# Kernel tuning notes

Measured on AMD Instinct MI355X. Metric: run time of the kernel, lower is better.

## Reference

```python
import jax, jax.numpy as jnp
import numpy as np

N_NODES = 100000
N_EDGES = 1600000
D_IN = 128
D_HID = 128
D_OUT = 128


def setup_inputs() -> dict:
    key = jax.random.key(0)
    ks = jax.random.split(key, 6)
    node_features = jax.random.normal(ks[0], (N_NODES, D_IN), dtype=jnp.float32)
    edge_index = jax.random.randint(ks[1], (2, N_EDGES), 0, N_NODES, dtype=jnp.int32)
    s1 = 1.0 / np.sqrt(D_IN)
    s2 = 1.0 / np.sqrt(D_HID)
    W1 = jax.random.normal(ks[2], (D_IN, D_HID), dtype=jnp.float32) * s1
    W2 = jax.random.normal(ks[3], (D_HID, D_HID), dtype=jnp.float32) * s2
    W3 = jax.random.normal(ks[4], (D_HID, D_OUT), dtype=jnp.float32) * s2
    b1 = jnp.zeros((D_HID,), dtype=jnp.float32)
    b2 = jnp.zeros((D_HID,), dtype=jnp.float32)
    b3 = jnp.zeros((D_OUT,), dtype=jnp.float32)
    return {"node_features": node_features, "edge_index": edge_index,
            "W1": W1, "b1": b1, "W2": W2, "b2": b2, "W3": W3, "b3": b3}


def _aggregate(x, src, dst, n_nodes):
    # mean over incoming neighbors (by dst), residual add; degree clamped to >=1
    msg = jax.ops.segment_sum(x[src], dst, num_segments=n_nodes)  # [N, D]
    deg = jax.ops.segment_sum(jnp.ones_like(dst, dtype=x.dtype), dst,
                              num_segments=n_nodes)
    deg = jnp.maximum(deg, 1.0)[:, None]
    return x + msg / deg


def reference(node_features, edge_index, W1, b1, W2, b2, W3, b3):
    n_nodes = node_features.shape[0]
    src, dst = edge_index[0], edge_index[1]
    x = _aggregate(node_features, src, dst, n_nodes)
    x = jax.nn.relu(x @ W1 + b1)
    x = _aggregate(x, src, dst, n_nodes)
    x = jax.nn.relu(x @ W2 + b2)
    x = x.mean(axis=0)  # graph readout -> [D_HID]
    return x @ W3 + b3  # [D_OUT]
```

## Files before the change

### kernel.cpp

```cpp
#include <hip/hip_runtime.h>

#define D 128
#define SLOTS 64
#define NB 391
#define BINCAP 5120
#define BATCH 2048
#define EPB 8
#define CNTSTRIDE 16
#define WPITCH 136

typedef __attribute__((ext_vector_type(8))) short short8;
typedef __attribute__((ext_vector_type(4))) float float4v;

__device__ inline unsigned short f2bf(float f) {
    union { float f; unsigned u; } a; a.f = f;
    unsigned u = a.u;
    return (unsigned short)((u + 0x7fffu + ((u >> 16) & 1u)) >> 16);
}
__device__ inline unsigned packbf(float a, float b) {
    return (unsigned)f2bf(a) | ((unsigned)f2bf(b) << 16);
}
__device__ inline unsigned pack4fp8(float a, float b, float c, float d) {
    int t = __builtin_amdgcn_cvt_pk_fp8_f32(a, b, 0, false);
    t = __builtin_amdgcn_cvt_pk_fp8_f32(c, d, t, true);
    return (unsigned)t;
}
__device__ inline unsigned char pack1fp8(float a) {
    int t = __builtin_amdgcn_cvt_pk_fp8_f32(a, 0.f, 0, false);
    return (unsigned char)(t & 0xff);
}
__device__ inline void acc8fp8(float* acc, uint2 w) {
    auto f0 = __builtin_amdgcn_cvt_pk_f32_fp8(w.x, false);
    auto f1 = __builtin_amdgcn_cvt_pk_f32_fp8(w.x, true);
    auto f2 = __builtin_amdgcn_cvt_pk_f32_fp8(w.y, false);
    auto f3 = __builtin_amdgcn_cvt_pk_f32_fp8(w.y, true);
    acc[0] += f0[0]; acc[1] += f0[1]; acc[2] += f1[0]; acc[3] += f1[1];
    acc[4] += f2[0]; acc[5] += f2[1]; acc[6] += f3[0]; acc[7] += f3[1];
}


__global__ __launch_bounds__(256) void k_head(const int* __restrict__ src,
                                              const int* __restrict__ dst, int nE,
                                              int* __restrict__ gcnt, int* __restrict__ bins,
                                              const float* __restrict__ x,
                                              unsigned char* __restrict__ y8,
                                              unsigned char* __restrict__ h8dummy,
                                              float* __restrict__ colsum,
                                              int n4, int nBatches) {
    __shared__ int hist[512];
    __shared__ int scan[512];
    __shared__ int base[NB];
    __shared__ int stage[BATCH];
    __shared__ int gofs[BATCH];
    int tid = threadIdx.x;

    if (blockIdx.x >= nBatches) {
        int cb = blockIdx.x - nBatches;
        if (cb == 0 && tid < 128) colsum[tid] = 0.f;
        int i = cb * 256 + tid;
        if (i >= n4 + 32) return;
        unsigned o8;
        if (i < n4) {
            float4 v = reinterpret_cast<const float4*>(x)[i];
            o8 = pack4fp8(v.x, v.y, v.z, v.w);
        } else {
            o8 = 0;
            reinterpret_cast<unsigned*>(h8dummy)[i - n4] = 0;
        }
        reinterpret_cast<unsigned*>(y8)[i] = o8;
        return;
    }

    int start = blockIdx.x * BATCH;
    int cntB = nE - start; if (cntB > BATCH) cntB = BATCH;
    if (cntB <= 0) return;

    hist[tid] = 0; hist[tid + 256] = 0;
    __syncthreads();

    int b[EPB], r[EPB], v[EPB];
    #pragma unroll
    for (int i = 0; i < EPB; ++i) {
        int e = start + i * 256 + tid;
        if (e < nE) {
            int d = dst[e];
            b[i] = d >> 8;
            v[i] = (src[e] << 8) | (d & 255);
            r[i] = atomicAdd(&hist[b[i]], 1);
        } else b[i] = -1;
    }
    __syncthreads();

    scan[tid] = hist[tid]; scan[tid + 256] = hist[tid + 256];
    __syncthreads();
    #pragma unroll
    for (int off = 1; off < 512; off <<= 1) {
        int v0 = (tid >= off) ? scan[tid - off] : 0;
        int v1 = (tid + 256 >= off) ? scan[tid + 256 - off] : 0;
        __syncthreads();
        scan[tid] += v0; scan[tid + 256] += v1;
        __syncthreads();
    }
    if (tid < 256 && tid < NB) base[tid] = atomicAdd(&gcnt[tid * CNTSTRIDE], hist[tid]);
    if (tid + 256 < NB) base[tid + 256] = atomicAdd(&gcnt[(tid + 256) * CNTSTRIDE], hist[tid + 256]);
    __syncthreads();

    #pragma unroll
    for (int i = 0; i < EPB; ++i) {
        if (b[i] >= 0) {
            int p = scan[b[i]] - hist[b[i]] + r[i];
            int o = base[b[i]] + r[i];
            stage[p] = v[i];
            gofs[p] = (o < BINCAP) ? (b[i] * BINCAP + o) : -1;
        }
    }
    __syncthreads();

    #pragma unroll
    for (int i = 0; i < EPB; ++i) {
        int p = i * 256 + tid;
        if (p < cntB) {
            int g = gofs[p];
            if (g >= 0) bins[g] = stage[p];
        }
    }
}


__global__ __launch_bounds__(256) void k_scatter2(const int* __restrict__ gcnt,
                                                  const int* __restrict__ bins,
                                                  int* __restrict__ slots,
                                                  int* __restrict__ deg, int n, int nAll) {
    __shared__ int slotsL[128 * SLOTS];
    __shared__ int cntL[128];
    int tid = threadIdx.x;
    int bin = blockIdx.x >> 1;
    int half = blockIdx.x & 1;
    if (tid < 128) cntL[tid] = 0;
    __syncthreads();

    int c = gcnt[bin * CNTSTRIDE]; if (c > BINCAP) c = BINCAP;
    const int* eb = bins + (size_t)bin * BINCAP;
    for (int i = tid; i < c; i += 256) {
        int v = eb[i];
        int dl = v & 255;
        if ((dl >> 7) == half) {
            int p = atomicAdd(&cntL[dl & 127], 1);
            if (p < SLOTS) slotsL[(dl & 127) * SLOTS + p] = v >> 8;
        }
    }
    __syncthreads();

    int node0 = bin * 256 + half * 128;
    int remNodes = n - node0;
    if (remNodes > 128) remNodes = 128;
    if (remNodes < 0) remNodes = 0;

    if (tid < remNodes) {
        int dg = cntL[tid]; if (dg > SLOTS) dg = SLOTS;
        int dgr = (dg + 3) & ~3;
        for (int p = dg; p < dgr; ++p) slotsL[tid * SLOTS + p] = nAll;
        deg[node0 + tid] = dg;
    }
    __syncthreads();

    uint4* gout = reinterpret_cast<uint4*>(slots + (size_t)node0 * SLOTS);
    const uint4* lin = reinterpret_cast<const uint4*>(slotsL);
    int nv = remNodes * SLOTS / 4;
    for (int i = tid; i < nv; i += 256) gout[i] = lin[i];
}


__global__ void k_agg(const unsigned char* __restrict__ Xin8,
                      unsigned short* __restrict__ Xout,
                      const int* __restrict__ deg, const int* __restrict__ slots, int n) {
    int t = blockIdx.x * 256 + threadIdx.x;
    int node = t >> 4;
    int lane = t & 15;
    if (node >= n) return;
    int dg = deg[node];
    int cnt4 = (dg + 3) & ~3;
    float acc[8] = {0.f, 0.f, 0.f, 0.f, 0.f, 0.f, 0.f, 0.f};
    const int* sl = slots + (size_t)node * SLOTS;
    for (int j = 0; j < cnt4; j += 4) {
        int4 s4 = *reinterpret_cast<const int4*>(sl + j);
        uint2 w0 = *reinterpret_cast<const uint2*>(Xin8 + (size_t)s4.x * D + lane * 8);
        uint2 w1 = *reinterpret_cast<const uint2*>(Xin8 + (size_t)s4.y * D + lane * 8);
        uint2 w2 = *reinterpret_cast<const uint2*>(Xin8 + (size_t)s4.z * D + lane * 8);
        uint2 w3 = *reinterpret_cast<const uint2*>(Xin8 + (size_t)s4.w * D + lane * 8);
        acc8fp8(acc, w0); acc8fp8(acc, w1); acc8fp8(acc, w2); acc8fp8(acc, w3);
    }
    float inv = 1.0f / (float)(dg > 0 ? dg : 1);
    uint2 s8 = *reinterpret_cast<const uint2*>(Xin8 + (size_t)node * D + lane * 8);
    float self[8] = {0.f, 0.f, 0.f, 0.f, 0.f, 0.f, 0.f, 0.f};
    acc8fp8(self, s8);
    float o[8];
    #pragma unroll
    for (int k = 0; k < 8; ++k) o[k] = self[k] + acc[k] * inv;
    uint4 ov;
    ov.x = packbf(o[0], o[1]); ov.y = packbf(o[2], o[3]);
    ov.z = packbf(o[4], o[5]); ov.w = packbf(o[6], o[7]);
    reinterpret_cast<uint4*>(Xout + (size_t)node * D)[lane] = ov;
}


__global__ __launch_bounds__(256) void k_gemm(const unsigned short* __restrict__ X,
                                              const float* __restrict__ W,
                                              const float* __restrict__ bias,
                                              unsigned char* __restrict__ Y8,
                                              float* __restrict__ colsum,
                                              int n, int mode) {
    __shared__ unsigned short Wt[128 * WPITCH];
    __shared__ float cs[128];
    int tid = threadIdx.x;
    int wave = tid >> 6, L = tid & 63;
    int m16 = L & 15, g = L >> 4;

    #pragma unroll
    for (int i = 0; i < 8; ++i) {
        int p = i * 256 + tid;
        int col = p & 127, kg = p >> 7;
        unsigned pk[4];
        #pragma unroll
        for (int h = 0; h < 4; ++h) {
            float w0 = W[(kg * 8 + 2 * h + 0) * 128 + col];
            float w1 = W[(kg * 8 + 2 * h + 1) * 128 + col];
            pk[h] = packbf(w0, w1);
        }
        *reinterpret_cast<uint4*>(&Wt[col * WPITCH + kg * 8]) =
            make_uint4(pk[0], pk[1], pk[2], pk[3]);
    }
    if (mode && tid < 128) cs[tid] = 0.f;
    __syncthreads();

    int row0 = blockIdx.x * 128 + wave * 32;
    float4v zero4 = {0.f, 0.f, 0.f, 0.f};
    float4v acc[2][8];
    #pragma unroll
    for (int rt = 0; rt < 2; ++rt)
        #pragma unroll
        for (int ct = 0; ct < 8; ++ct) acc[rt][ct] = zero4;

    #pragma unroll
    for (int q = 0; q < 4; ++q) {
        int k0 = q * 32;
        short8 a[2];
        #pragma unroll
        for (int rt = 0; rt < 2; ++rt) {
            int row = row0 + rt * 16 + m16;
            short8 af = {0, 0, 0, 0, 0, 0, 0, 0};
            if (row < n)
                af = *reinterpret_cast<const short8*>(X + (size_t)row * D + k0 + g * 8);
            a[rt] = af;
        }
        #pragma unroll
        for (int ct = 0; ct < 8; ++ct) {
            short8 b = *reinterpret_cast<const short8*>(&Wt[(ct * 16 + m16) * WPITCH + k0 + g * 8]);
            acc[0][ct] = __builtin_amdgcn_mfma_f32_16x16x32_bf16(a[0], b, acc[0][ct], 0, 0, 0);
            acc[1][ct] = __builtin_amdgcn_mfma_f32_16x16x32_bf16(a[1], b, acc[1][ct], 0, 0, 0);
        }
    }

    float bj[8];
    #pragma unroll
    for (int ct = 0; ct < 8; ++ct) bj[ct] = bias[ct * 16 + m16];

    if (mode == 0) {
        #pragma unroll
        for (int rt = 0; rt < 2; ++rt)
            #pragma unroll
            for (int i = 0; i < 4; ++i) {
                int row = row0 + rt * 16 + g * 4 + i;
                if (row < n) {
                    #pragma unroll
                    for (int ct = 0; ct < 8; ++ct) {
                        float v = fmaxf(acc[rt][ct][i] + bj[ct], 0.f);
                        Y8[(size_t)row * D + ct * 16 + m16] = pack1fp8(v);
                    }
                }
            }
    } else {
        float csv[8] = {0.f, 0.f, 0.f, 0.f, 0.f, 0.f, 0.f, 0.f};
        #pragma unroll
        for (int rt = 0; rt < 2; ++rt)
            #pragma unroll
            for (int i = 0; i < 4; ++i) {
                int row = row0 + rt * 16 + g * 4 + i;
                if (row < n) {
                    #pragma unroll
                    for (int ct = 0; ct < 8; ++ct)
                        csv[ct] += fmaxf(acc[rt][ct][i] + bj[ct], 0.f);
                }
            }
        #pragma unroll
        for (int ct = 0; ct < 8; ++ct) atomicAdd(&cs[ct * 16 + m16], csv[ct]);
        __syncthreads();
        if (tid < 128) atomicAdd(&colsum[tid], cs[tid]);
    }
}


__global__ void k_final(const float* __restrict__ colsum, const float* __restrict__ W3,
                        const float* __restrict__ b3, float* __restrict__ out, float invN) {
    int j = threadIdx.x;
    float acc = b3[j];
    #pragma unroll 8
    for (int k = 0; k < D; ++k)
        acc += colsum[k] * invN * W3[k * D + j];
    out[j] = acc;
}


extern "C" void kernel_launch(void* const* d_in, const int* in_sizes, int n_in,
                              void* d_out, int out_size, void* d_ws, size_t ws_size,
                              hipStream_t stream) {
    const float* nf = (const float*)d_in[0];
    const int*   ei = (const int*)d_in[1];
    const float* W1 = (const float*)d_in[2];
    const float* b1 = (const float*)d_in[3];
    const float* W2 = (const float*)d_in[4];
    const float* b2 = (const float*)d_in[5];
    const float* W3 = (const float*)d_in[6];
    const float* b3 = (const float*)d_in[7];
    float* out = (float*)d_out;

    int n  = in_sizes[0] / D;
    int nE = in_sizes[1] / 2;
    const int* src = ei;
    const int* dst = ei + nE;

    int nBins = (n + 255) / 256;
    int nBatches = (nE + BATCH - 1) / BATCH;
    int n4 = n * D / 4;

    char* ws = (char*)d_ws;
    size_t off = 0;
    auto alloc = [&](size_t bytes) -> void* {
        off = (off + 255) & ~(size_t)255;
        void* p = ws + off;
        off += bytes;
        return p;
    };
    int* gcnt  = (int*)alloc((size_t)nBins * CNTSTRIDE * 4);
    int* bins  = (int*)alloc((size_t)nBins * BINCAP * 4);
    int* slots = (int*)alloc((size_t)nBins * 256 * SLOTS * 4);
    int* deg   = (int*)alloc((size_t)n * 4);
    unsigned char*  x8  = (unsigned char*) alloc((size_t)(n + 1) * D);
    unsigned short* t16 = (unsigned short*)alloc((size_t)n * D * 2);
    unsigned char*  h8  = (unsigned char*) alloc((size_t)(n + 1) * D);
    float* colsum = (float*)alloc(128 * 4);

    hipMemsetAsync(gcnt, 0, (size_t)nBins * CNTSTRIDE * 4, stream);

    int gC = (n4 + 32 + 255) / 256;
    int gA = (n * 16 + 255) / 256;
    int gG = (n + 127) / 128;

    k_head<<<nBatches + gC, 256, 0, stream>>>(src, dst, nE, gcnt, bins,
                                              nf, x8, h8 + (size_t)n * D,
                                              colsum, n4, nBatches);
    k_scatter2<<<nBins * 2, 256, 0, stream>>>(gcnt, bins, slots, deg, n, n);

    k_agg<<<gA, 256, 0, stream>>>(x8, t16, deg, slots, n);
    k_gemm<<<gG, 256, 0, stream>>>(t16, W1, b1, h8, (float*)nullptr, n, 0);
    k_agg<<<gA, 256, 0, stream>>>(h8, t16, deg, slots, n);
    k_gemm<<<gG, 256, 0, stream>>>(t16, W2, b2, (unsigned char*)nullptr, colsum, n, 1);
    k_final<<<1, 128, 0, stream>>>(colsum, W3, b3, out, 1.0f / (float)n);
}
```

Baseline: 275.0 us.

## Reorder GEMM before aggregation and fuse bias/ReLU/readout into aggregation

Uses the linearity of mean aggregation to compute X@W before gathering neighbours, since (x + mean(x_nbr))W = xW + mean(x_nbr W). Bias, ReLU and, for the second layer, the column-sum readout then move into the aggregation kernel. The first GEMM reads the fp32 input directly, which removes the separate fp8 conversion pass and drops the head kernel's conversion blocks. It also replaces the partition kernel's shared-memory Hillis-Steele scan with a wave shuffle scan. The trade-off is that neighbour features are now gathered as fp8 products of the GEMM rather than fp8 inputs, which changes rounding error, and the readout now does per-lane shared-memory atomics inside the aggregation kernel.

After: 397.9 us. 44.7% more time.

```diff
diff --git a/kernel.cpp b/kernel.cpp
--- a/kernel.cpp
+++ b/kernel.cpp
@@ -20,11 +20,6 @@
 __device__ inline unsigned packbf(float a, float b) {
     return (unsigned)f2bf(a) | ((unsigned)f2bf(b) << 16);
 }
-__device__ inline unsigned pack4fp8(float a, float b, float c, float d) {
-    int t = __builtin_amdgcn_cvt_pk_fp8_f32(a, b, 0, false);
-    t = __builtin_amdgcn_cvt_pk_fp8_f32(c, d, t, true);
-    return (unsigned)t;
-}
 __device__ inline unsigned char pack1fp8(float a) {
     int t = __builtin_amdgcn_cvt_pk_fp8_f32(a, 0.f, 0, false);
     return (unsigned char)(t & 0xff);
@@ -39,36 +34,22 @@
 }
 
 
-__global__ __launch_bounds__(256) void k_head(const int* __restrict__ src,
+__global__ __launch_bounds__(256) void k_part(const int* __restrict__ src,
                                               const int* __restrict__ dst, int nE,
                                               int* __restrict__ gcnt, int* __restrict__ bins,
-                                              const float* __restrict__ x,
-                                              unsigned char* __restrict__ y8,
-                                              unsigned char* __restrict__ h8dummy,
-                                              float* __restrict__ colsum,
-                                              int n4, int nBatches) {
+                                              unsigned char* __restrict__ y8dummy,
+                                              float* __restrict__ colsum) {
     __shared__ int hist[512];
-    __shared__ int scan[512];
+    __shared__ int excl[512];
     __shared__ int base[NB];
     __shared__ int stage[BATCH];
     __shared__ int gofs[BATCH];
+    __shared__ int waveSum[4];
     int tid = threadIdx.x;
 
-    if (blockIdx.x >= nBatches) {
-        int cb = blockIdx.x - nBatches;
-        if (cb == 0 && tid < 128) colsum[tid] = 0.f;
-        int i = cb * 256 + tid;
-        if (i >= n4 + 32) return;
-        unsigned o8;
-        if (i < n4) {
-            float4 v = reinterpret_cast<const float4*>(x)[i];
-            o8 = pack4fp8(v.x, v.y, v.z, v.w);
-        } else {
-            o8 = 0;
-            reinterpret_cast<unsigned*>(h8dummy)[i - n4] = 0;
-        }
-        reinterpret_cast<unsigned*>(y8)[i] = o8;
-        return;
+    if (blockIdx.x == 0) {
+        if (tid < 32) reinterpret_cast<unsigned*>(y8dummy)[tid] = 0;
+        if (tid < 128) colsum[tid] = 0.f;
     }
 
     int start = blockIdx.x * BATCH;
@@ -91,24 +72,33 @@
     }
     __syncthreads();
 
-    scan[tid] = hist[tid]; scan[tid + 256] = hist[tid + 256];
-    __syncthreads();
-    #pragma unroll
-    for (int off = 1; off < 512; off <<= 1) {
-        int v0 = (tid >= off) ? scan[tid - off] : 0;
-        int v1 = (tid + 256 >= off) ? scan[tid + 256 - off] : 0;
-        __syncthreads();
-        scan[tid] += v0; scan[tid + 256] += v1;
-        __syncthreads();
-    }
-    if (tid < 256 && tid < NB) base[tid] = atomicAdd(&gcnt[tid * CNTSTRIDE], hist[tid]);
+    int e0 = tid * 2, e1 = e0 + 1;
+    int h0 = hist[e0], h1v = hist[e1];
+    int s = h0 + h1v;
+    int lane = tid & 63, w = tid >> 6;
+    int sum = s;
+    #pragma unroll
+    for (int off2 = 1; off2 < 64; off2 <<= 1) {
+        int tmp = __shfl_up(sum, off2, 64);
+        if (lane >= off2) sum += tmp;
+    }
+    if (lane == 63) waveSum[w] = sum;
+    __syncthreads();
+    int wbase = 0;
+    if (w > 0) wbase += waveSum[0];
+    if (w > 1) wbase += waveSum[1];
+    if (w > 2) wbase += waveSum[2];
+    int exclPair = wbase + sum - s;
+    excl[e0] = exclPair;
+    excl[e1] = exclPair + h0;
+    if (tid < NB) base[tid] = atomicAdd(&gcnt[tid * CNTSTRIDE], hist[tid]);
     if (tid + 256 < NB) base[tid + 256] = atomicAdd(&gcnt[(tid + 256) * CNTSTRIDE], hist[tid + 256]);
     __syncthreads();
 
     #pragma unroll
     for (int i = 0; i < EPB; ++i) {
         if (b[i] >= 0) {
-            int p = scan[b[i]] - hist[b[i]] + r[i];
+            int p = excl[b[i]] + r[i];
             int o = base[b[i]] + r[i];
             stage[p] = v[i];
             gofs[p] = (o < BINCAP) ? (b[i] * BINCAP + o) : -1;
@@ -171,47 +161,10 @@
 }
 
 
-__global__ void k_agg(const unsigned char* __restrict__ Xin8,
-                      unsigned short* __restrict__ Xout,
-                      const int* __restrict__ deg, const int* __restrict__ slots, int n) {
-    int t = blockIdx.x * 256 + threadIdx.x;
-    int node = t >> 4;
-    int lane = t & 15;
-    if (node >= n) return;
-    int dg = deg[node];
-    int cnt4 = (dg + 3) & ~3;
-    float acc[8] = {0.f, 0.f, 0.f, 0.f, 0.f, 0.f, 0.f, 0.f};
-    const int* sl = slots + (size_t)node * SLOTS;
-    for (int j = 0; j < cnt4; j += 4) {
-        int4 s4 = *reinterpret_cast<const int4*>(sl + j);
-        uint2 w0 = *reinterpret_cast<const uint2*>(Xin8 + (size_t)s4.x * D + lane * 8);
-        uint2 w1 = *reinterpret_cast<const uint2*>(Xin8 + (size_t)s4.y * D + lane * 8);
-        uint2 w2 = *reinterpret_cast<const uint2*>(Xin8 + (size_t)s4.z * D + lane * 8);
-        uint2 w3 = *reinterpret_cast<const uint2*>(Xin8 + (size_t)s4.w * D + lane * 8);
-        acc8fp8(acc, w0); acc8fp8(acc, w1); acc8fp8(acc, w2); acc8fp8(acc, w3);
-    }
-    float inv = 1.0f / (float)(dg > 0 ? dg : 1);
-    uint2 s8 = *reinterpret_cast<const uint2*>(Xin8 + (size_t)node * D + lane * 8);
-    float self[8] = {0.f, 0.f, 0.f, 0.f, 0.f, 0.f, 0.f, 0.f};
-    acc8fp8(self, s8);
-    float o[8];
-    #pragma unroll
-    for (int k = 0; k < 8; ++k) o[k] = self[k] + acc[k] * inv;
-    uint4 ov;
-    ov.x = packbf(o[0], o[1]); ov.y = packbf(o[2], o[3]);
-    ov.z = packbf(o[4], o[5]); ov.w = packbf(o[6], o[7]);
-    reinterpret_cast<uint4*>(Xout + (size_t)node * D)[lane] = ov;
-}
-
-
-__global__ __launch_bounds__(256) void k_gemm(const unsigned short* __restrict__ X,
+__global__ __launch_bounds__(256) void k_gemm(const void* __restrict__ Xv, int xfp32,
                                               const float* __restrict__ W,
-                                              const float* __restrict__ bias,
-                                              unsigned char* __restrict__ Y8,
-                                              float* __restrict__ colsum,
-                                              int n, int mode) {
+                                              unsigned char* __restrict__ Y8, int n) {
     __shared__ unsigned short Wt[128 * WPITCH];
-    __shared__ float cs[128];
     int tid = threadIdx.x;
     int wave = tid >> 6, L = tid & 63;
     int m16 = L & 15, g = L >> 4;
@@ -230,7 +183,6 @@
         *reinterpret_cast<uint4*>(&Wt[col * WPITCH + kg * 8]) =
             make_uint4(pk[0], pk[1], pk[2], pk[3]);
     }
-    if (mode && tid < 128) cs[tid] = 0.f;
     __syncthreads();
 
     int row0 = blockIdx.x * 128 + wave * 32;
@@ -249,8 +201,19 @@
         for (int rt = 0; rt < 2; ++rt) {
             int row = row0 + rt * 16 + m16;
             short8 af = {0, 0, 0, 0, 0, 0, 0, 0};
-            if (row < n)
-                af = *reinterpret_cast<const short8*>(X + (size_t)row * D + k0 + g * 8);
+            if (row < n) {
+                if (xfp32) {
+                    const float* Xf = (const float*)Xv;
+                    float4 p0 = *reinterpret_cast<const float4*>(Xf + (size_t)row * D + k0 + g * 8);
+                    float4 p1 = *reinterpret_cast<const float4*>(Xf + (size_t)row * D + k0 + g * 8 + 4);
+                    uint4 u = make_uint4(packbf(p0.x, p0.y), packbf(p0.z, p0.w),
+                                         packbf(p1.x, p1.y), packbf(p1.z, p1.w));
+                    af = *reinterpret_cast<short8*>(&u);
+                } else {
+                    const unsigned short* Xh = (const unsigned short*)Xv;
+                    af = *reinterpret_cast<const short8*>(Xh + (size_t)row * D + k0 + g * 8);
+                }
+            }
             a[rt] = af;
         }
         #pragma unroll
@@ -261,39 +224,66 @@
         }
     }
 
-    float bj[8];
-    #pragma unroll
-    for (int ct = 0; ct < 8; ++ct) bj[ct] = bias[ct * 16 + m16];
-
-    if (mode == 0) {
-        #pragma unroll
-        for (int rt = 0; rt < 2; ++rt)
-            #pragma unroll
-            for (int i = 0; i < 4; ++i) {
-                int row = row0 + rt * 16 + g * 4 + i;
-                if (row < n) {
-                    #pragma unroll
-                    for (int ct = 0; ct < 8; ++ct) {
-                        float v = fmaxf(acc[rt][ct][i] + bj[ct], 0.f);
-                        Y8[(size_t)row * D + ct * 16 + m16] = pack1fp8(v);
-                    }
-                }
+    #pragma unroll
+    for (int rt = 0; rt < 2; ++rt)
+        #pragma unroll
+        for (int i = 0; i < 4; ++i) {
+            int row = row0 + rt * 16 + g * 4 + i;
+            if (row < n) {
+                #pragma unroll
+                for (int ct = 0; ct < 8; ++ct)
+                    Y8[(size_t)row * D + ct * 16 + m16] = pack1fp8(acc[rt][ct][i]);
             }
-    } else {
-        float csv[8] = {0.f, 0.f, 0.f, 0.f, 0.f, 0.f, 0.f, 0.f};
-        #pragma unroll
-        for (int rt = 0; rt < 2; ++rt)
-            #pragma unroll
-            for (int i = 0; i < 4; ++i) {
-                int row = row0 + rt * 16 + g * 4 + i;
-                if (row < n) {
-                    #pragma unroll
-                    for (int ct = 0; ct < 8; ++ct)
-                        csv[ct] += fmaxf(acc[rt][ct][i] + bj[ct], 0.f);
-                }
-            }
-        #pragma unroll
-        for (int ct = 0; ct < 8; ++ct) atomicAdd(&cs[ct * 16 + m16], csv[ct]);
+        }
+}
+
+
+__global__ void k_agg(const unsigned char* __restrict__ Y8,
+                      const float* __restrict__ bias,
+                      unsigned short* __restrict__ Hout,
+                      float* __restrict__ colsum,
+                      const int* __restrict__ deg, const int* __restrict__ slots,
+                      int n, int mode) {
+    __shared__ float cs[128];
+    int tid = threadIdx.x;
+    int t = blockIdx.x * 256 + tid;
+    int node = t >> 4;
+    int lane = t & 15;
+    if (mode && tid < 128) cs[tid] = 0.f;
+    if (mode) __syncthreads();
+
+    float o[8] = {0.f, 0.f, 0.f, 0.f, 0.f, 0.f, 0.f, 0.f};
+    if (node < n) {
+        int dg = deg[node];
+        int cnt4 = (dg + 3) & ~3;
+        float acc[8] = {0.f, 0.f, 0.f, 0.f, 0.f, 0.f, 0.f, 0.f};
+        const int* sl = slots + (size_t)node * SLOTS;
+        for (int j = 0; j < cnt4; j += 4) {
+            int4 s4 = *reinterpret_cast<const int4*>(sl + j);
+            uint2 w0 = *reinterpret_cast<const uint2*>(Y8 + (size_t)s4.x * D + lane * 8);
+            uint2 w1 = *reinterpret_cast<const uint2*>(Y8 + (size_t)s4.y * D + lane * 8);
+            uint2 w2 = *reinterpret_cast<const uint2*>(Y8 + (size_t)s4.z * D + lane * 8);
+            uint2 w3 = *reinterpret_cast<const uint2*>(Y8 + (size_t)s4.w * D + lane * 8);
+            acc8fp8(acc, w0); acc8fp8(acc, w1); acc8fp8(acc, w2); acc8fp8(acc, w3);
+        }
+        float inv = 1.0f / (float)(dg > 0 ? dg : 1);
+        uint2 s8 = *reinterpret_cast<const uint2*>(Y8 + (size_t)node * D + lane * 8);
+        float self[8] = {0.f, 0.f, 0.f, 0.f, 0.f, 0.f, 0.f, 0.f};
+        acc8fp8(self, s8);
+        #pragma unroll
+        for (int k = 0; k < 8; ++k)
+            o[k] = fmaxf(self[k] + acc[k] * inv + bias[lane * 8 + k], 0.f);
+
+        if (mode == 0) {
+            uint4 ov;
+            ov.x = packbf(o[0], o[1]); ov.y = packbf(o[2], o[3]);
+            ov.z = packbf(o[4], o[5]); ov.w = packbf(o[6], o[7]);
+            reinterpret_cast<uint4*>(Hout + (size_t)node * D)[lane] = ov;
+        }
+    }
+    if (mode) {
+        #pragma unroll
+        for (int k = 0; k < 8; ++k) atomicAdd(&cs[lane * 8 + k], o[k]);
         __syncthreads();
         if (tid < 128) atomicAdd(&colsum[tid], cs[tid]);
     }
@@ -331,7 +321,6 @@
 
     int nBins = (n + 255) / 256;
     int nBatches = (nE + BATCH - 1) / BATCH;
-    int n4 = n * D / 4;
 
     char* ws = (char*)d_ws;
     size_t off = 0;
@@ -345,25 +334,22 @@
     int* bins  = (int*)alloc((size_t)nBins * BINCAP * 4);
     int* slots = (int*)alloc((size_t)nBins * 256 * SLOTS * 4);
     int* deg   = (int*)alloc((size_t)n * 4);
-    unsigned char*  x8  = (unsigned char*) alloc((size_t)(n + 1) * D);
-    unsigned short* t16 = (unsigned short*)alloc((size_t)n * D * 2);
-    unsigned char*  h8  = (unsigned char*) alloc((size_t)(n + 1) * D);
+    unsigned char*  y8 = (unsigned char*) alloc((size_t)(n + 1) * D);
+    unsigned short* h1 = (unsigned short*)alloc((size_t)n * D * 2);
     float* colsum = (float*)alloc(128 * 4);
 
     hipMemsetAsync(gcnt, 0, (size_t)nBins * CNTSTRIDE * 4, stream);
 
-    int gC = (n4 + 32 + 255) / 256;
     int gA = (n * 16 + 255) / 256;
     int gG = (n + 127) / 128;
 
-    k_head<<<nBatches + gC, 256, 0, stream>>>(src, dst, nE, gcnt, bins,
-                                              nf, x8, h8 + (size_t)n * D,
-                                              colsum, n4, nBatches);
+    k_part<<<nBatches, 256, 0, stream>>>(src, dst, nE, gcnt, bins,
+                                         y8 + (size_t)n * D, colsum);
+    k_gemm<<<gG, 256, 0, stream>>>(nf, 1, W1, y8, n);
     k_scatter2<<<nBins * 2, 256, 0, stream>>>(gcnt, bins, slots, deg, n, n);
 
-    k_agg<<<gA, 256, 0, stream>>>(x8, t16, deg, slots, n);
-    k_gemm<<<gG, 256, 0, stream>>>(t16, W1, b1, h8, (float*)nullptr, n, 0);
-    k_agg<<<gA, 256, 0, stream>>>(h8, t16, deg, slots, n);
-    k_gemm<<<gG, 256, 0, stream>>>(t16, W2, b2, (unsigned char*)nullptr, colsum, n, 1);
+    k_agg<<<gA, 256, 0, stream>>>(y8, b1, h1, (float*)nullptr, deg, slots, n, 0);
+    k_gemm<<<gG, 256, 0, stream>>>(h1, 0, W2, y8, n);
+    k_agg<<<gA, 256, 0, stream>>>(y8, b2, (unsigned short*)nullptr, colsum, deg, slots, n, 1);
     k_final<<<1, 128, 0, stream>>>(colsum, W3, b3, out, 1.0f / (float)n);
 }
```
